# Optimization experiments

Hardware: AMD Instinct MI355X
Metric: run time of the kernel (lower is better)

Reference implementation:

```python
import jax, jax.numpy as jnp
import numpy as np

F = 845   # feature_num
P = 39    # field_num
K = 32    # implicit_vector_dim
B = 32768 # batch


def _field_ids():
    # feature_to_field(n) = n if n < 13 else (n - 13) // K + 13
    n = np.arange(F)
    return np.where(n < 13, n, (n - 13) // K + 13).astype(np.int32)


def setup_inputs() -> dict:
    key = jax.random.key(0)
    k0, k1, k2, k3 = jax.random.split(key, 4)
    # scale inputs/params down so the quadratic term does not saturate sigmoid
    X = jax.random.normal(k0, (B, F), jnp.float32) * 0.05
    field_matrix = jax.random.normal(k1, (F, P, K), jnp.float32) * 0.1
    a = jax.random.normal(k2, (F, F), jnp.float32)
    w_lin = jax.random.normal(k3, (F, 1), jnp.float32) * 0.02
    b_lin = jnp.zeros((1,), jnp.float32)
    return {"X": X, "field_matrix": field_matrix, "a": a,
            "w_lin": w_lin, "b_lin": b_lin}


def reference(X, field_matrix, a, w_lin, b_lin):
    # The original loop computes, per feature i:
    #   result[b] += X[b, i] * sum_j a[i, j] * X[b, j]
    #                * <field_matrix[i, field(i)], field_matrix[j, field(j)]>
    # i.e. a batched quadratic form X W X^T (diagonal) with
    #   W[i, j] = a[i, j] * (V @ V.T)[i, j],  V[i] = field_matrix[i, field(i)].
    fid = jnp.asarray(_field_ids())
    V = field_matrix[jnp.arange(F), fid]        # [F, K] own-field vectors
    W = a * (V @ V.T)                           # [F, F]
    quad = jnp.sum((X @ W) * X, axis=-1)        # [B]
    lin = X @ w_lin[:, 0] + b_lin[0]            # [B]
    # original casts to double at the end; we stay in float32 (math identical)
    return jax.nn.sigmoid(lin + quad)
```

## Files before the change

kernel.cpp:

```cpp
#include <hip/hip_runtime.h>
#include <hip/hip_bf16.h>
#include <math.h>

typedef unsigned short ushort_t;
typedef unsigned int   uint_t;

typedef __attribute__((ext_vector_type(8))) __bf16 bf16x8;
typedef __attribute__((ext_vector_type(4))) float  f32x4;

#define BATCH 32768
#define FDIM  845
#define FP    896
#define KT    27
#define NBLK  7
#define MBLK  256

__device__ __forceinline__ int fld(int n) { return (n < 13) ? n : (((n - 13) >> 5) + 13); }

__device__ __forceinline__ ushort_t f2bf(float f) {
    uint_t u = __builtin_bit_cast(uint_t, f);
    uint_t r = u + 0x7FFFu + ((u >> 16) & 1u);
    return (ushort_t)(r >> 16);
}
__device__ __forceinline__ float bf2f(ushort_t h) {
    uint_t u = ((uint_t)h) << 16;
    return __builtin_bit_cast(float, u);
}

__device__ __forceinline__ void gload_lds16(const ushort_t* g, ushort_t* l) {
    __builtin_amdgcn_global_load_lds(
        (const __attribute__((address_space(1))) void*)g,
        (__attribute__((address_space(3))) void*)l, 16, 0, 0);
}

__global__ void conv_x(const float* __restrict__ X, ushort_t* __restrict__ Xb) {
    uint_t p   = blockIdx.x * 256 + threadIdx.x;
    uint_t row = p / 448;
    uint_t c0  = (p % 448) * 2;
    ushort_t v[2];
    #pragma unroll
    for (int j = 0; j < 2; ++j) {
        uint_t c = c0 + j;
        float f = (c < FDIM) ? X[(size_t)row * FDIM + c] : (c == FDIM ? 1.0f : 0.0f);
        v[j] = f2bf(f);
    }
    *(ushort2*)&Xb[(size_t)row * FP + c0] = make_ushort2(v[0], v[1]);
}

__global__ void gather_v(const float* __restrict__ fm, ushort_t* __restrict__ Vb) {
    int idx = blockIdx.x * 256 + threadIdx.x;
    int row = idx >> 5, k = idx & 31;
    float v = (row < FDIM) ? fm[(size_t)(row * 39 + fld(row)) * 32 + k] : 0.0f;
    Vb[idx] = f2bf(v);
}

__global__ __launch_bounds__(256, 2)
void prep_w(const float* __restrict__ a, const float* __restrict__ wl,
            const ushort_t* __restrict__ Vb, ushort_t* __restrict__ WbT) {
    __shared__ float As[64 * 65];
    const int bx = blockIdx.x;
    const int i0 = (bx % 14) * 64, j0 = (bx / 14) * 64;
    const int tid  = threadIdx.x;
    const int wave = tid >> 6, lane = tid & 63;
    const int l15  = lane & 15, l4 = lane >> 4;

    {
        const int row = tid >> 2, seg = tid & 3;
        const int gi  = i0 + row;
        #pragma unroll
        for (int q = 0; q < 16; ++q) {
            const int jl = seg * 16 + q, gj = j0 + jl;
            float v = (gi < FDIM && gj < FDIM) ? a[(size_t)gi * FDIM + gj] : 0.0f;
            As[row * 65 + jl] = v;
        }
    }

    bf16x8 af = *(const bf16x8*)&Vb[(size_t)(j0 + wave * 16 + l15) * 32 + l4 * 8];
    f32x4 acc[4];
    #pragma unroll
    for (int it = 0; it < 4; ++it) {
        bf16x8 bf = *(const bf16x8*)&Vb[(size_t)(i0 + it * 16 + l15) * 32 + l4 * 8];
        acc[it] = __builtin_amdgcn_mfma_f32_16x16x32_bf16(af, bf, (f32x4){0.f,0.f,0.f,0.f}, 0, 0, 0);
    }
    __syncthreads();

    #pragma unroll
    for (int it = 0; it < 4; ++it) {
        #pragma unroll
        for (int r = 0; r < 4; ++r) {
            const int jl = wave * 16 + l4 * 4 + r;
            const int il = it * 16 + l15;
            const int gi = i0 + il, gj = j0 + jl;
            float w = acc[it][r] * As[il * 65 + jl];
            if (gj == FDIM) w = (gi < FDIM) ? wl[gi] : 0.0f;
            WbT[(size_t)gj * FP + gi] = f2bf(w);
        }
    }
}

__global__ __launch_bounds__(256, 2)
void ffm_gemm(const ushort_t* __restrict__ Xb, const ushort_t* __restrict__ WbT,
              float* __restrict__ qpart) {
    __shared__ ushort_t As[128 * 32];
    __shared__ ushort_t Bs[128 * 32];

    const int tid  = threadIdx.x;
    const int wave = tid >> 6, lane = tid & 63;
    const int l15  = lane & 15, l4 = lane >> 4;
    const int wm   = wave >> 1, wn = wave & 1;

    const int bid  = blockIdx.x;
    const int xcd  = bid & 7;
    const int slot = bid >> 3;
    const int nb   = slot % 7;
    const int m0   = (xcd * 32 + slot / 7) * 128;
    const int n0   = nb * 128;

    const int srow  = lane >> 2;
    const int kslot = lane & 3;

    f32x4 acc[4][4];
    #pragma unroll
    for (int i = 0; i < 4; ++i)
        #pragma unroll
        for (int j = 0; j < 4; ++j) acc[i][j] = (f32x4){0.f, 0.f, 0.f, 0.f};

    for (int kt = 0; kt < KT; ++kt) {
        const int k0 = kt * 32;
        __syncthreads();
        #pragma unroll
        for (int half = 0; half < 2; ++half) {
            const int row = wave * 32 + half * 16 + srow;
            const int ksg = kslot ^ ((row >> 1) & 3);
            gload_lds16(Xb  + (size_t)(m0 + row) * FP + k0 + ksg * 8,
                        &As[(wave * 32 + half * 16) * 32]);
            gload_lds16(WbT + (size_t)(n0 + row) * FP + k0 + ksg * 8,
                        &Bs[(wave * 32 + half * 16) * 32]);
        }
        __syncthreads();

        bf16x8 af[4], bfv[4];
        #pragma unroll
        for (int i = 0; i < 4; ++i) {
            const int r = wm * 64 + i * 16 + l15;
            const int s = l4 ^ ((r >> 1) & 3);
            af[i] = *(const bf16x8*)&As[r * 32 + s * 8];
        }
        #pragma unroll
        for (int j = 0; j < 4; ++j) {
            const int r = wn * 64 + j * 16 + l15;
            const int s = l4 ^ ((r >> 1) & 3);
            bfv[j] = *(const bf16x8*)&Bs[r * 32 + s * 8];
        }
        #pragma unroll
        for (int i = 0; i < 4; ++i)
            #pragma unroll
            for (int j = 0; j < 4; ++j)
                acc[i][j] = __builtin_amdgcn_mfma_f32_16x16x32_bf16(af[i], bfv[j], acc[i][j], 0, 0, 0);
    }

    float q[4][4] = {};
    #pragma unroll
    for (int i = 0; i < 4; ++i)
        #pragma unroll
        for (int j = 0; j < 4; ++j) {
            const int col = n0 + wn * 64 + j * 16 + l15;
            #pragma unroll
            for (int r = 0; r < 4; ++r) {
                const int row = m0 + wm * 64 + i * 16 + l4 * 4 + r;
                q[i][r] += acc[i][j][r] * bf2f(Xb[(size_t)row * FP + col]);
            }
        }
    #pragma unroll
    for (int off = 1; off < 16; off <<= 1)
        #pragma unroll
        for (int i = 0; i < 4; ++i)
            #pragma unroll
            for (int r = 0; r < 4; ++r) q[i][r] += __shfl_xor(q[i][r], off, 64);

    if (l15 == 0) {
        float* dst = qpart + (size_t)(nb * 2 + wn) * BATCH;
        #pragma unroll
        for (int i = 0; i < 4; ++i)
            #pragma unroll
            for (int r = 0; r < 4; ++r)
                dst[m0 + wm * 64 + i * 16 + l4 * 4 + r] = q[i][r];
    }
}

__global__ void finish(const float* __restrict__ qpart, const float* __restrict__ blin,
                       float* __restrict__ out) {
    int b = blockIdx.x * 256 + threadIdx.x;
    float s = blin[0];
    #pragma unroll
    for (int p = 0; p < 14; ++p) s += qpart[(size_t)p * BATCH + b];
    out[b] = 1.0f / (1.0f + expf(-s));
}

extern "C" void kernel_launch(void* const* d_in, const int* in_sizes, int n_in,
                              void* d_out, int out_size, void* d_ws, size_t ws_size,
                              hipStream_t stream) {
    const float* X  = (const float*)d_in[0];
    const float* fm = (const float*)d_in[1];
    const float* a  = (const float*)d_in[2];
    const float* wl = (const float*)d_in[3];
    const float* bl = (const float*)d_in[4];
    float* out = (float*)d_out;

    char* ws = (char*)d_ws;
    ushort_t* Xb    = (ushort_t*)ws;
    ushort_t* WbT   = (ushort_t*)(ws + 58720256);
    ushort_t* Vb    = (ushort_t*)(ws + 60325888);
    float*    qpart = (float*)   (ws + 60383232);

    conv_x  <<<(BATCH * 448) / 256, 256, 0, stream>>>(X, Xb);
    gather_v<<<(FP * 32) / 256,     256, 0, stream>>>(fm, Vb);
    prep_w  <<<14 * 14,             256, 0, stream>>>(a, wl, Vb, WbT);
    ffm_gemm<<<MBLK * NBLK,         256, 0, stream>>>(Xb, WbT, qpart);
    finish  <<<BATCH / 256,         256, 0, stream>>>(qpart, bl, out);
}
```

Baseline: 250.6 us.

## Double GEMM K-tile to 64, fuse V gather into prep_w, widen conv_x

The GEMM main loop now stages 64-wide K slices per iteration with an 8-way XOR swizzle, which halves the number of barrier-separated load phases at the cost of doubled LDS use. The separate gather_v kernel is removed and the own-field vectors are gathered straight into shared memory inside prep_w, saving one launch and a global round trip. conv_x now has each thread convert 16 columns and write them with two 16-byte stores instead of 2-element stores, cutting thread count and store count. Changing K from 27x32 to 14x64 reads padded columns up to 896, which matches FP.

```diff
diff --git a/kernel.cpp b/kernel.cpp
--- a/kernel.cpp
+++ b/kernel.cpp
@@ -11,7 +11,7 @@
 #define BATCH 32768
 #define FDIM  845
 #define FP    896
-#define KT    27
+#define KT    14
 #define NBLK  7
 #define MBLK  256
 
@@ -35,29 +35,27 @@
 
 __global__ void conv_x(const float* __restrict__ X, ushort_t* __restrict__ Xb) {
     uint_t p   = blockIdx.x * 256 + threadIdx.x;
-    uint_t row = p / 448;
-    uint_t c0  = (p % 448) * 2;
-    ushort_t v[2];
-    #pragma unroll
-    for (int j = 0; j < 2; ++j) {
+    uint_t row = p / 56;
+    uint_t c0  = (p % 56) * 16;
+    const float* xp = X + (size_t)row * FDIM;
+    union { ushort_t u[16]; uint4 v[2]; } pk;
+    #pragma unroll
+    for (int j = 0; j < 16; ++j) {
         uint_t c = c0 + j;
-        float f = (c < FDIM) ? X[(size_t)row * FDIM + c] : (c == FDIM ? 1.0f : 0.0f);
-        v[j] = f2bf(f);
-    }
-    *(ushort2*)&Xb[(size_t)row * FP + c0] = make_ushort2(v[0], v[1]);
-}
-
-__global__ void gather_v(const float* __restrict__ fm, ushort_t* __restrict__ Vb) {
-    int idx = blockIdx.x * 256 + threadIdx.x;
-    int row = idx >> 5, k = idx & 31;
-    float v = (row < FDIM) ? fm[(size_t)(row * 39 + fld(row)) * 32 + k] : 0.0f;
-    Vb[idx] = f2bf(v);
+        float f = (c < FDIM) ? xp[c] : (c == FDIM ? 1.0f : 0.0f);
+        pk.u[j] = f2bf(f);
+    }
+    uint4* dst = (uint4*)&Xb[(size_t)row * FP + c0];
+    dst[0] = pk.v[0];
+    dst[1] = pk.v[1];
 }
 
 __global__ __launch_bounds__(256, 2)
-void prep_w(const float* __restrict__ a, const float* __restrict__ wl,
-            const ushort_t* __restrict__ Vb, ushort_t* __restrict__ WbT) {
-    __shared__ float As[64 * 65];
+void prep_w(const float* __restrict__ fm, const float* __restrict__ a,
+            const float* __restrict__ wl, ushort_t* __restrict__ WbT) {
+    __shared__ float    As[64 * 65];
+    __shared__ ushort_t Vi[64 * 32];
+    __shared__ ushort_t Vj[64 * 32];
     const int bx = blockIdx.x;
     const int i0 = (bx % 14) * 64, j0 = (bx / 14) * 64;
     const int tid  = threadIdx.x;
@@ -65,6 +63,22 @@
     const int l15  = lane & 15, l4 = lane >> 4;
 
     {
+        const int row = tid >> 2;
+        const int kq  = (tid & 3) * 8;
+        union { ushort_t u[8]; uint4 v; } pi, pj;
+        const int gi = i0 + row, gj = j0 + row;
+        #pragma unroll
+        for (int q = 0; q < 8; ++q) {
+            float vi = 0.0f, vj = 0.0f;
+            if (gi < FDIM) vi = fm[(size_t)(gi * 39 + fld(gi)) * 32 + kq + q];
+            if (gj < FDIM) vj = fm[(size_t)(gj * 39 + fld(gj)) * 32 + kq + q];
+            pi.u[q] = f2bf(vi);
+            pj.u[q] = f2bf(vj);
+        }
+        *(uint4*)&Vi[row * 32 + kq] = pi.v;
+        *(uint4*)&Vj[row * 32 + kq] = pj.v;
+    }
+    {
         const int row = tid >> 2, seg = tid & 3;
         const int gi  = i0 + row;
         #pragma unroll
@@ -74,15 +88,15 @@
             As[row * 65 + jl] = v;
         }
     }
-
-    bf16x8 af = *(const bf16x8*)&Vb[(size_t)(j0 + wave * 16 + l15) * 32 + l4 * 8];
+    __syncthreads();
+
+    bf16x8 af = *(const bf16x8*)&Vj[(wave * 16 + l15) * 32 + l4 * 8];
     f32x4 acc[4];
     #pragma unroll
     for (int it = 0; it < 4; ++it) {
-        bf16x8 bf = *(const bf16x8*)&Vb[(size_t)(i0 + it * 16 + l15) * 32 + l4 * 8];
+        bf16x8 bf = *(const bf16x8*)&Vi[(it * 16 + l15) * 32 + l4 * 8];
         acc[it] = __builtin_amdgcn_mfma_f32_16x16x32_bf16(af, bf, (f32x4){0.f,0.f,0.f,0.f}, 0, 0, 0);
     }
-    __syncthreads();
 
     #pragma unroll
     for (int it = 0; it < 4; ++it) {
@@ -101,8 +115,8 @@
 __global__ __launch_bounds__(256, 2)
 void ffm_gemm(const ushort_t* __restrict__ Xb, const ushort_t* __restrict__ WbT,
               float* __restrict__ qpart) {
-    __shared__ ushort_t As[128 * 32];
-    __shared__ ushort_t Bs[128 * 32];
+    __shared__ ushort_t As[128 * 64];
+    __shared__ ushort_t Bs[128 * 64];
 
     const int tid  = threadIdx.x;
     const int wave = tid >> 6, lane = tid & 63;
@@ -116,8 +130,8 @@
     const int m0   = (xcd * 32 + slot / 7) * 128;
     const int n0   = nb * 128;
 
-    const int srow  = lane >> 2;
-    const int kslot = lane & 3;
+    const int r8 = lane >> 3;
+    const int s8 = lane & 7;
 
     f32x4 acc[4][4];
     #pragma unroll
@@ -126,37 +140,45 @@
         for (int j = 0; j < 4; ++j) acc[i][j] = (f32x4){0.f, 0.f, 0.f, 0.f};
 
     for (int kt = 0; kt < KT; ++kt) {
-        const int k0 = kt * 32;
+        const int k0 = kt * 64;
         __syncthreads();
         #pragma unroll
-        for (int half = 0; half < 2; ++half) {
-            const int row = wave * 32 + half * 16 + srow;
-            const int ksg = kslot ^ ((row >> 1) & 3);
-            gload_lds16(Xb  + (size_t)(m0 + row) * FP + k0 + ksg * 8,
-                        &As[(wave * 32 + half * 16) * 32]);
-            gload_lds16(WbT + (size_t)(n0 + row) * FP + k0 + ksg * 8,
-                        &Bs[(wave * 32 + half * 16) * 32]);
+        for (int h = 0; h < 4; ++h) {
+            const int row = wave * 32 + h * 8 + r8;
+            const int sg  = s8 ^ (row & 7);
+            gload_lds16(Xb  + (size_t)(m0 + row) * FP + k0 + sg * 8,
+                        &As[(wave * 32 + h * 8) * 64]);
+            gload_lds16(WbT + (size_t)(n0 + row) * FP + k0 + sg * 8,
+                        &Bs[(wave * 32 + h * 8) * 64]);
         }
         __syncthreads();
 
-        bf16x8 af[4], bfv[4];
+        bf16x8 af[4][2], bfv[4][2];
         #pragma unroll
         for (int i = 0; i < 4; ++i) {
             const int r = wm * 64 + i * 16 + l15;
-            const int s = l4 ^ ((r >> 1) & 3);
-            af[i] = *(const bf16x8*)&As[r * 32 + s * 8];
+            #pragma unroll
+            for (int h = 0; h < 2; ++h) {
+                const int s = (h * 4 + l4) ^ (r & 7);
+                af[i][h] = *(const bf16x8*)&As[r * 64 + s * 8];
+            }
         }
         #pragma unroll
         for (int j = 0; j < 4; ++j) {
             const int r = wn * 64 + j * 16 + l15;
-            const int s = l4 ^ ((r >> 1) & 3);
-            bfv[j] = *(const bf16x8*)&Bs[r * 32 + s * 8];
+            #pragma unroll
+            for (int h = 0; h < 2; ++h) {
+                const int s = (h * 4 + l4) ^ (r & 7);
+                bfv[j][h] = *(const bf16x8*)&Bs[r * 64 + s * 8];
+            }
         }
         #pragma unroll
         for (int i = 0; i < 4; ++i)
             #pragma unroll
-            for (int j = 0; j < 4; ++j)
-                acc[i][j] = __builtin_amdgcn_mfma_f32_16x16x32_bf16(af[i], bfv[j], acc[i][j], 0, 0, 0);
+            for (int j = 0; j < 4; ++j) {
+                acc[i][j] = __builtin_amdgcn_mfma_f32_16x16x32_bf16(af[i][0], bfv[j][0], acc[i][j], 0, 0, 0);
+                acc[i][j] = __builtin_amdgcn_mfma_f32_16x16x32_bf16(af[i][1], bfv[j][1], acc[i][j], 0, 0, 0);
+            }
     }
 
     float q[4][4] = {};
@@ -210,12 +232,10 @@
     char* ws = (char*)d_ws;
     ushort_t* Xb    = (ushort_t*)ws;
     ushort_t* WbT   = (ushort_t*)(ws + 58720256);
-    ushort_t* Vb    = (ushort_t*)(ws + 60325888);
     float*    qpart = (float*)   (ws + 60383232);
 
-    conv_x  <<<(BATCH * 448) / 256, 256, 0, stream>>>(X, Xb);
-    gather_v<<<(FP * 32) / 256,     256, 0, stream>>>(fm, Vb);
-    prep_w  <<<14 * 14,             256, 0, stream>>>(a, wl, Vb, WbT);
-    ffm_gemm<<<MBLK * NBLK,         256, 0, stream>>>(Xb, WbT, qpart);
-    finish  <<<BATCH / 256,         256, 0, stream>>>(qpart, bl, out);
-}
+    conv_x  <<<(BATCH * 56) / 256, 256, 0, stream>>>(X, Xb);
+    prep_w  <<<14 * 14,            256, 0, stream>>>(fm, a, wl, WbT);
+    ffm_gemm<<<MBLK * NBLK,        256, 0, stream>>>(Xb, WbT, qpart);
+    finish  <<<BATCH / 256,        256, 0, stream>>>(qpart, bl, out);
+}
```

After: 262.0 us. 4.6% more time.
